# Kernel tuning notes

Measured on AMD Instinct MI355X. Metric: run time of the kernel, lower is better.

Reference implementation:

```python
import jax, jax.numpy as jnp
import numpy as np

N, M, D, DV = 8192, 8192, 64, 64

def setup_inputs() -> dict:
    key = jax.random.key(0)
    kq, kk, kv = jax.random.split(key, 3)
    Q = jax.random.normal(kq, (N, D), dtype=jnp.float32)
    K = jax.random.normal(kk, (M, D), dtype=jnp.float32)
    V = jax.random.normal(kv, (M, DV), dtype=jnp.float32)
    return {"Q": Q, "K": K, "V": V}

def reference(Q, K, V):
    d = K.shape[-1]
    scores = jnp.einsum('nd,md->nm', Q, K) / jnp.sqrt(jnp.float32(d))  # [N, M]
    attn = jax.nn.softmax(scores, axis=-1)
    return attn @ V  # [N, DV]
```

## Files before the change

kernel.cpp:

```cpp
#include <hip/hip_runtime.h>


#define NQ 8192
#define NK 8192

typedef float f32x4 __attribute__((ext_vector_type(4)));
typedef short short8 __attribute__((ext_vector_type(8)));
union U4 { uint4 u; short8 s; };

#define MFMA16 __builtin_amdgcn_mfma_f32_16x16x32_bf16

__device__ __forceinline__ unsigned pk2(float a, float b) {
    unsigned ua = __builtin_bit_cast(unsigned, a);
    unsigned ub = __builtin_bit_cast(unsigned, b);
    ua = (ua + 0x7FFFu + ((ua >> 16) & 1u)) >> 16;
    ub = (ub + 0x7FFFu + ((ub >> 16) & 1u)) & 0xFFFF0000u;
    return ua | ub;
}

__device__ __forceinline__ unsigned pkt(float a, float b) {
    return __builtin_amdgcn_perm(__builtin_bit_cast(unsigned, b),
                                 __builtin_bit_cast(unsigned, a), 0x07060302u);
}

__global__ __launch_bounds__(256)
void prepass(const float* __restrict__ Kg, const float* __restrict__ Vg,
             uint4* __restrict__ Kb4, uint4* __restrict__ Vt4) {
    __shared__ float ld[64 * 33];
    const int t = threadIdx.x, b = blockIdx.x;

    if (b < 256) {
        const int kl = t >> 3, dg = t & 7;
        const int e = kl & 1, i16 = kl >> 1, h = dg >> 2, q = dg & 3;
        const float* gp = Kg + (size_t)(b * 32 + kl) * 64 + dg * 8;
        float4 f0 = *(const float4*)gp;
        float4 f1 = *(const float4*)(gp + 4);
        uint4 o = make_uint4(pk2(f0.x, f0.y), pk2(f0.z, f0.w),
                             pk2(f1.x, f1.y), pk2(f1.z, f1.w));
        Kb4[(size_t)(b * 4 + e * 2 + h) * 64 + i16 * 4 + q] = o;
    } else {
        const int c = b - 256;
        {
            const int key = t >> 3, dg = t & 7;
            const float* gp = Vg + (size_t)(c * 32 + key) * 64 + dg * 8;
            float4 f0 = *(const float4*)gp;
            float4 f1 = *(const float4*)(gp + 4);
            ld[(dg * 8 + 0) * 33 + key] = f0.x;
            ld[(dg * 8 + 1) * 33 + key] = f0.y;
            ld[(dg * 8 + 2) * 33 + key] = f0.z;
            ld[(dg * 8 + 3) * 33 + key] = f0.w;
            ld[(dg * 8 + 4) * 33 + key] = f1.x;
            ld[(dg * 8 + 5) * 33 + key] = f1.y;
            ld[(dg * 8 + 6) * 33 + key] = f1.z;
            ld[(dg * 8 + 7) * 33 + key] = f1.w;
        }
        __syncthreads();
        {
            const int dim = t >> 2, kq = t & 3;
            const int dt = dim >> 4, i16 = dim & 15;
            float v[8];
            #pragma unroll
            for (int j = 0; j < 8; ++j) v[j] = ld[dim * 33 + kq * 8 + j];
            uint4 o = make_uint4(pk2(v[0], v[1]), pk2(v[2], v[3]),
                                 pk2(v[4], v[5]), pk2(v[6], v[7]));
            Vt4[(size_t)(c * 4 + dt) * 64 + i16 * 4 + kq] = o;
        }
    }
}

__global__ __launch_bounds__(512, 1)
void attn_main(const float* __restrict__ Qg,
               const uint4* __restrict__ Kb4,
               const uint4* __restrict__ Vt4,
               float* __restrict__ Opart,
               float* __restrict__ Lpart) {
    __shared__ uint4 shb4[4160];
    float* sF = (float*)shb4;
    unsigned* shu = (unsigned*)shb4;

    const int t = threadIdx.x, w = t >> 6, lane = t & 63;
    const int q = lane >> 4, i16 = lane & 15;
    const int bid = blockIdx.x;
    const int kh = bid & 1;
    const int rg = bid >> 1;
    const int qb0 = rg * 64;
    const int lsl = i16 * 4 + q;
    const int phase = rg & 15;

    const int tpw = ((i16 >> 2) & 1) + 2 * q + 32 * (i16 >> 3);
    const int pp  = i16 & 3;
    const int tpr = (q & 1) + 2 * ((i16 >> 2) & 3) + 8 * (i16 & 3) + 32 * (q >> 1);

    uint4 kfA[4], vfA[4], kfB[4], vfB[4];

#define CBASE(TT) (((kh << 7) + ((((TT) + phase) & 15) * 8 + w)) * 4)

#define LOAD_K(KD, TT)                                                               \
    do {                                                                             \
        const int cb = CBASE(TT);                                                    \
        _Pragma("unroll")                                                            \
        for (int eh = 0; eh < 4; ++eh)                                               \
            (KD)[eh] = Kb4[(size_t)(cb + eh) * 64 + lsl];                            \
    } while (0)

#define LOAD_V(VD, TT)                                                               \
    do {                                                                             \
        const int cb = CBASE(TT);                                                    \
        _Pragma("unroll")                                                            \
        for (int dt = 0; dt < 4; ++dt)                                               \
            (VD)[dt] = Vt4[(size_t)(cb + dt) * 64 + lsl];                            \
    } while (0)

    LOAD_K(kfA, 0);
    LOAD_V(vfA, 0);
    LOAD_K(kfB, 1);

    const float SCL = 0.18033688011112042f;
    short8 aq[4][2];
    #pragma unroll
    for (int rt = 0; rt < 4; ++rt) {
        const float* qp = Qg + (size_t)(qb0 + rt * 16 + i16) * 64 + q * 8;
        float4 f0 = *(const float4*)(qp);
        float4 f1 = *(const float4*)(qp + 4);
        U4 u;
        u.u = make_uint4(pk2(f0.x * SCL, f0.y * SCL), pk2(f0.z * SCL, f0.w * SCL),
                         pk2(f1.x * SCL, f1.y * SCL), pk2(f1.z * SCL, f1.w * SCL));
        aq[rt][0] = u.s;
        f0 = *(const float4*)(qp + 32);
        f1 = *(const float4*)(qp + 36);
        u.u = make_uint4(pk2(f0.x * SCL, f0.y * SCL), pk2(f0.z * SCL, f0.w * SCL),
                         pk2(f1.x * SCL, f1.y * SCL), pk2(f1.z * SCL, f1.w * SCL));
        aq[rt][1] = u.s;
    }

    f32x4 acc[4][4];
    float lsum[4][4];
    #pragma unroll
    for (int rt = 0; rt < 4; ++rt) {
        #pragma unroll
        for (int dt = 0; dt < 4; ++dt) { acc[rt][dt][0]=0.f; acc[rt][dt][1]=0.f; acc[rt][dt][2]=0.f; acc[rt][dt][3]=0.f; }
        #pragma unroll
        for (int r = 0; r < 4; ++r) lsum[rt][r] = 0.f;
    }

#define QKEXP(KD, PAR)                                                               \
    do {                                                                             \
        _Pragma("unroll")                                                            \
        for (int rt = 0; rt < 4; ++rt) {                                             \
            f32x4 s0, s1;                                                            \
            s0[0]=-16.f; s0[1]=-16.f; s0[2]=-16.f; s0[3]=-16.f;                      \
            s1[0]=-16.f; s1[1]=-16.f; s1[2]=-16.f; s1[3]=-16.f;                      \
            U4 u0, u1, u2, u3;                                                       \
            u0.u = (KD)[0]; u1.u = (KD)[1]; u2.u = (KD)[2]; u3.u = (KD)[3];          \
            s0 = MFMA16(aq[rt][0], u0.s, s0, 0, 0, 0);                               \
            s0 = MFMA16(aq[rt][1], u1.s, s0, 0, 0, 0);                               \
            s1 = MFMA16(aq[rt][0], u2.s, s1, 0, 0, 0);                               \
            s1 = MFMA16(aq[rt][1], u3.s, s1, 0, 0, 0);                               \
            const int rbase = (((w * 4 + rt) * 2) + (PAR)) * 256;                    \
            _Pragma("unroll")                                                        \
            for (int r = 0; r < 4; ++r) {                                            \
                float p0 = __builtin_amdgcn_exp2f(s0[r]);                            \
                float p1 = __builtin_amdgcn_exp2f(s1[r]);                            \
                lsum[rt][r] += p0;                                                   \
                lsum[rt][r] += p1;                                                   \
                shu[rbase + (tpw + 8 * r) * 4 + pp] = pkt(p0, p1);                   \
            }                                                                        \
        }                                                                            \
    } while (0)

#define PVS(VD, PAR)                                                                 \
    do {                                                                             \
        U4 ap[4];                                                                    \
        _Pragma("unroll")                                                            \
        for (int rt = 0; rt < 4; ++rt)                                               \
            ap[rt].u = shb4[(((w * 4 + rt) * 2) + (PAR)) * 64 + tpr];                \
        _Pragma("unroll")                                                            \
        for (int dt = 0; dt < 4; ++dt) {                                             \
            U4 bv; bv.u = (VD)[dt];                                                  \
            _Pragma("unroll")                                                        \
            for (int rt = 0; rt < 4; ++rt)                                           \
                acc[rt][dt] = MFMA16(ap[rt].s, bv.s, acc[rt][dt], 0, 0, 0);          \
        }                                                                            \
    } while (0)

    QKEXP(kfA, 0);
    LOAD_K(kfA, 2);
    LOAD_V(vfB, 1);
    #pragma unroll 1
    for (int tt = 1; tt < 15; tt += 2) {
        QKEXP(kfB, 1);
        LOAD_K(kfB, tt + 2);
        PVS(vfA, 0);
        LOAD_V(vfA, tt + 1);
        QKEXP(kfA, 0);
        LOAD_K(kfA, tt + 3);
        PVS(vfB, 1);
        LOAD_V(vfB, tt + 2);
        __builtin_amdgcn_sched_barrier(0);
    }
    QKEXP(kfB, 1);
    PVS(vfA, 0);
    PVS(vfB, 1);

    #pragma unroll
    for (int rt = 0; rt < 4; ++rt)
        #pragma unroll
        for (int r = 0; r < 4; ++r) {
            float v = lsum[rt][r];
            v += __shfl_xor(v, 1);
            v += __shfl_xor(v, 2);
            v += __shfl_xor(v, 4);
            v += __shfl_xor(v, 8);
            lsum[rt][r] = v;
        }

    __syncthreads();
    for (int step = 4; step >= 1; step >>= 1) {
        if (w >= step && w < 2 * step) {
            float* base = sF + (w - step) * 4160;
            #pragma unroll
            for (int rt = 0; rt < 4; ++rt) {
                #pragma unroll
                for (int dt = 0; dt < 4; ++dt)
                    #pragma unroll
                    for (int r = 0; r < 4; ++r)
                        base[(rt * 16 + 4 * q + r) * 64 + dt * 16 + i16] = acc[rt][dt][r];
                if (i16 == 0) {
                    #pragma unroll
                    for (int r = 0; r < 4; ++r) base[4096 + rt * 16 + 4 * q + r] = lsum[rt][r];
                }
            }
        }
        __syncthreads();
        if (w < step) {
            const float* base = sF + w * 4160;
            #pragma unroll
            for (int rt = 0; rt < 4; ++rt) {
                #pragma unroll
                for (int dt = 0; dt < 4; ++dt)
                    #pragma unroll
                    for (int r = 0; r < 4; ++r)
                        acc[rt][dt][r] += base[(rt * 16 + 4 * q + r) * 64 + dt * 16 + i16];
                #pragma unroll
                for (int r = 0; r < 4; ++r) lsum[rt][r] += base[4096 + rt * 16 + 4 * q + r];
            }
        }
        __syncthreads();
    }

    if (w == 0) {
        #pragma unroll
        for (int rt = 0; rt < 4; ++rt) {
            #pragma unroll
            for (int dt = 0; dt < 4; ++dt)
                #pragma unroll
                for (int r = 0; r < 4; ++r) {
                    const int row = qb0 + rt * 16 + 4 * q + r;
                    Opart[((size_t)kh * 8192 + row) * 64 + dt * 16 + i16] = acc[rt][dt][r];
                }
            if (i16 == 0) {
                #pragma unroll
                for (int r = 0; r < 4; ++r)
                    Lpart[kh * 8192 + qb0 + rt * 16 + 4 * q + r] = lsum[rt][r];
            }
        }
    }
}

__global__ __launch_bounds__(256)
void merge(const float* __restrict__ Opart, const float* __restrict__ Lpart,
           float* __restrict__ Og) {
    const int idx = blockIdx.x * 256 + threadIdx.x;
    const int row = idx >> 4, seg = idx & 15;
    const float4 a = *(const float4*)(Opart + (size_t)row * 64 + seg * 4);
    const float4 b = *(const float4*)(Opart + ((size_t)8192 + row) * 64 + seg * 4);
    const float inv = 1.0f / (Lpart[row] + Lpart[8192 + row]);
    float4 o;
    o.x = (a.x + b.x) * inv;
    o.y = (a.y + b.y) * inv;
    o.z = (a.z + b.z) * inv;
    o.w = (a.w + b.w) * inv;
    *(float4*)(Og + (size_t)row * 64 + seg * 4) = o;
}

extern "C" void kernel_launch(void* const* d_in, const int* in_sizes, int n_in,
                              void* d_out, int out_size, void* d_ws, size_t ws_size,
                              hipStream_t stream) {
    const float* Q = (const float*)d_in[0];
    const float* K = (const float*)d_in[1];
    const float* V = (const float*)d_in[2];
    float* O = (float*)d_out;
    char* ws = (char*)d_ws;
    uint4* Kb4   = (uint4*)ws;
    uint4* Vt4   = (uint4*)(ws + (1 << 20));
    float* Opart = (float*)(ws + (2 << 20));
    float* Lpart = (float*)(ws + (6 << 20));
    hipLaunchKernelGGL(prepass, dim3(512), dim3(256), 0, stream, K, V, Kb4, Vt4);
    hipLaunchKernelGGL(attn_main, dim3(256), dim3(512), 0, stream, Q, Kb4, Vt4, Opart, Lpart);
    hipLaunchKernelGGL(merge, dim3(512), dim3(256), 0, stream, Opart, Lpart, O);
}
```

Baseline: 90.37 us.

## Compute transposed scores and shuffle P in registers instead of LDS

The QK product is computed as K·Q^T, so each lane holds scores for one query row. The exp'd probabilities are rearranged into the PV A-operand layout with permlane swap instructions, replacing the LDS write/read round trip. The K and V prepass layouts change to match, and the pipeline is simplified so each tile does QK, exp and PV in one step. This removes LDS traffic and its latency, but the fused per-tile dependency chain may hide less latency than the old split schedule.

```diff
diff --git a/kernel.cpp b/kernel.cpp
--- a/kernel.cpp
+++ b/kernel.cpp
@@ -30,14 +30,16 @@
     const int t = threadIdx.x, b = blockIdx.x;
 
     if (b < 256) {
-        const int kl = t >> 3, dg = t & 7;
-        const int e = kl & 1, i16 = kl >> 1, h = dg >> 2, q = dg & 3;
-        const float* gp = Kg + (size_t)(b * 32 + kl) * 64 + dg * 8;
+        const int f = t >> 6, l = t & 63;
+        const int i16 = l & 15, g = l >> 4;
+        const int row = b * 32 + (f >> 1) * 16 + i16;
+        const int dg = g + (f & 1) * 4;
+        const float* gp = Kg + (size_t)row * 64 + dg * 8;
         float4 f0 = *(const float4*)gp;
         float4 f1 = *(const float4*)(gp + 4);
         uint4 o = make_uint4(pk2(f0.x, f0.y), pk2(f0.z, f0.w),
                              pk2(f1.x, f1.y), pk2(f1.z, f1.w));
-        Kb4[(size_t)(b * 4 + e * 2 + h) * 64 + i16 * 4 + q] = o;
+        Kb4[(size_t)(b * 4 + f) * 64 + l] = o;
     } else {
         const int c = b - 256;
         {
@@ -63,7 +65,7 @@
             for (int j = 0; j < 8; ++j) v[j] = ld[dim * 33 + kq * 8 + j];
             uint4 o = make_uint4(pk2(v[0], v[1]), pk2(v[2], v[3]),
                                  pk2(v[4], v[5]), pk2(v[6], v[7]));
-            Vt4[(size_t)(c * 4 + dt) * 64 + i16 * 4 + kq] = o;
+            Vt4[(size_t)(c * 4 + dt) * 64 + kq * 16 + i16] = o;
         }
     }
 }
@@ -74,9 +76,7 @@
                const uint4* __restrict__ Vt4,
                float* __restrict__ Opart,
                float* __restrict__ Lpart) {
-    __shared__ uint4 shb4[4160];
-    float* sF = (float*)shb4;
-    unsigned* shu = (unsigned*)shb4;
+    __shared__ float sF[4 * 4160];
 
     const int t = threadIdx.x, w = t >> 6, lane = t & 63;
     const int q = lane >> 4, i16 = lane & 15;
@@ -84,12 +84,7 @@
     const int kh = bid & 1;
     const int rg = bid >> 1;
     const int qb0 = rg * 64;
-    const int lsl = i16 * 4 + q;
     const int phase = rg & 15;
-
-    const int tpw = ((i16 >> 2) & 1) + 2 * q + 32 * (i16 >> 3);
-    const int pp  = i16 & 3;
-    const int tpr = (q & 1) + 2 * ((i16 >> 2) & 3) + 8 * (i16 & 3) + 32 * (q >> 1);
 
     uint4 kfA[4], vfA[4], kfB[4], vfB[4];
 
@@ -99,8 +94,8 @@
     do {                                                                             \
         const int cb = CBASE(TT);                                                    \
         _Pragma("unroll")                                                            \
-        for (int eh = 0; eh < 4; ++eh)                                               \
-            (KD)[eh] = Kb4[(size_t)(cb + eh) * 64 + lsl];                            \
+        for (int f = 0; f < 4; ++f)                                                  \
+            (KD)[f] = Kb4[(size_t)(cb + f) * 64 + lane];                             \
     } while (0)
 
 #define LOAD_V(VD, TT)                                                               \
@@ -108,12 +103,11 @@
         const int cb = CBASE(TT);                                                    \
         _Pragma("unroll")                                                            \
         for (int dt = 0; dt < 4; ++dt)                                               \
-            (VD)[dt] = Vt4[(size_t)(cb + dt) * 64 + lsl];                            \
+            (VD)[dt] = Vt4[(size_t)(cb + dt) * 64 + lane];                           \
     } while (0)
 
-    LOAD_K(kfA, 0);
-    LOAD_V(vfA, 0);
-    LOAD_K(kfB, 1);
+    LOAD_K(kfA, 0); LOAD_V(vfA, 0);
+    LOAD_K(kfB, 1); LOAD_V(vfB, 1);
 
     const float SCL = 0.18033688011112042f;
     short8 aq[4][2];
@@ -134,85 +128,69 @@
     }
 
     f32x4 acc[4][4];
-    float lsum[4][4];
+    float lsum[4];
     #pragma unroll
     for (int rt = 0; rt < 4; ++rt) {
         #pragma unroll
         for (int dt = 0; dt < 4; ++dt) { acc[rt][dt][0]=0.f; acc[rt][dt][1]=0.f; acc[rt][dt][2]=0.f; acc[rt][dt][3]=0.f; }
-        #pragma unroll
-        for (int r = 0; r < 4; ++r) lsum[rt][r] = 0.f;
-    }
-
-#define QKEXP(KD, PAR)                                                               \
+        lsum[rt] = 0.f;
+    }
+
+#define TILE(KD, VD)                                                                 \
     do {                                                                             \
         _Pragma("unroll")                                                            \
         for (int rt = 0; rt < 4; ++rt) {                                             \
             f32x4 s0, s1;                                                            \
             s0[0]=-16.f; s0[1]=-16.f; s0[2]=-16.f; s0[3]=-16.f;                      \
             s1[0]=-16.f; s1[1]=-16.f; s1[2]=-16.f; s1[3]=-16.f;                      \
-            U4 u0, u1, u2, u3;                                                       \
-            u0.u = (KD)[0]; u1.u = (KD)[1]; u2.u = (KD)[2]; u3.u = (KD)[3];          \
-            s0 = MFMA16(aq[rt][0], u0.s, s0, 0, 0, 0);                               \
-            s0 = MFMA16(aq[rt][1], u1.s, s0, 0, 0, 0);                               \
-            s1 = MFMA16(aq[rt][0], u2.s, s1, 0, 0, 0);                               \
-            s1 = MFMA16(aq[rt][1], u3.s, s1, 0, 0, 0);                               \
-            const int rbase = (((w * 4 + rt) * 2) + (PAR)) * 256;                    \
+            U4 k0, k1, k2, k3;                                                       \
+            k0.u = (KD)[0]; k1.u = (KD)[1]; k2.u = (KD)[2]; k3.u = (KD)[3];          \
+            s0 = MFMA16(k0.s, aq[rt][0], s0, 0, 0, 0);                               \
+            s0 = MFMA16(k1.s, aq[rt][1], s0, 0, 0, 0);                               \
+            s1 = MFMA16(k2.s, aq[rt][0], s1, 0, 0, 0);                               \
+            s1 = MFMA16(k3.s, aq[rt][1], s1, 0, 0, 0);                               \
+            float p00 = __builtin_amdgcn_exp2f(s0[0]);                               \
+            float p01 = __builtin_amdgcn_exp2f(s0[1]);                               \
+            float p02 = __builtin_amdgcn_exp2f(s0[2]);                               \
+            float p03 = __builtin_amdgcn_exp2f(s0[3]);                               \
+            float p10 = __builtin_amdgcn_exp2f(s1[0]);                               \
+            float p11 = __builtin_amdgcn_exp2f(s1[1]);                               \
+            float p12 = __builtin_amdgcn_exp2f(s1[2]);                               \
+            float p13 = __builtin_amdgcn_exp2f(s1[3]);                               \
+            lsum[rt] += ((p00 + p01) + (p02 + p03)) + ((p10 + p11) + (p12 + p13));   \
+            unsigned w0 = pkt(p00, p01), w1 = pkt(p02, p03);                         \
+            unsigned w2 = pkt(p10, p11), w3 = pkt(p12, p13);                         \
+            asm("v_permlane32_swap_b32 %0, %1" : "+v"(w0), "+v"(w2));                \
+            asm("v_permlane16_swap_b32 %0, %1" : "+v"(w0), "+v"(w2));                \
+            asm("v_permlane32_swap_b32 %0, %1" : "+v"(w1), "+v"(w3));                \
+            asm("v_permlane16_swap_b32 %0, %1" : "+v"(w1), "+v"(w3));                \
+            U4 ap; ap.u = make_uint4(w0, w1, w2, w3);                                \
             _Pragma("unroll")                                                        \
-            for (int r = 0; r < 4; ++r) {                                            \
-                float p0 = __builtin_amdgcn_exp2f(s0[r]);                            \
-                float p1 = __builtin_amdgcn_exp2f(s1[r]);                            \
-                lsum[rt][r] += p0;                                                   \
-                lsum[rt][r] += p1;                                                   \
-                shu[rbase + (tpw + 8 * r) * 4 + pp] = pkt(p0, p1);                   \
+            for (int dt = 0; dt < 4; ++dt) {                                         \
+                U4 bv; bv.u = (VD)[dt];                                              \
+                acc[rt][dt] = MFMA16(ap.s, bv.s, acc[rt][dt], 0, 0, 0);              \
             }                                                                        \
         }                                                                            \
     } while (0)
 
-#define PVS(VD, PAR)                                                                 \
-    do {                                                                             \
-        U4 ap[4];                                                                    \
-        _Pragma("unroll")                                                            \
-        for (int rt = 0; rt < 4; ++rt)                                               \
-            ap[rt].u = shb4[(((w * 4 + rt) * 2) + (PAR)) * 64 + tpr];                \
-        _Pragma("unroll")                                                            \
-        for (int dt = 0; dt < 4; ++dt) {                                             \
-            U4 bv; bv.u = (VD)[dt];                                                  \
-            _Pragma("unroll")                                                        \
-            for (int rt = 0; rt < 4; ++rt)                                           \
-                acc[rt][dt] = MFMA16(ap[rt].s, bv.s, acc[rt][dt], 0, 0, 0);          \
-        }                                                                            \
-    } while (0)
-
-    QKEXP(kfA, 0);
-    LOAD_K(kfA, 2);
-    LOAD_V(vfB, 1);
     #pragma unroll 1
-    for (int tt = 1; tt < 15; tt += 2) {
-        QKEXP(kfB, 1);
-        LOAD_K(kfB, tt + 2);
-        PVS(vfA, 0);
-        LOAD_V(vfA, tt + 1);
-        QKEXP(kfA, 0);
-        LOAD_K(kfA, tt + 3);
-        PVS(vfB, 1);
-        LOAD_V(vfB, tt + 2);
+    for (int tt = 0; tt < 14; tt += 2) {
+        TILE(kfA, vfA);
+        LOAD_K(kfA, tt + 2); LOAD_V(vfA, tt + 2);
+        TILE(kfB, vfB);
+        LOAD_K(kfB, tt + 3); LOAD_V(vfB, tt + 3);
         __builtin_amdgcn_sched_barrier(0);
     }
-    QKEXP(kfB, 1);
-    PVS(vfA, 0);
-    PVS(vfB, 1);
+    TILE(kfA, vfA);
+    TILE(kfB, vfB);
 
     #pragma unroll
-    for (int rt = 0; rt < 4; ++rt)
-        #pragma unroll
-        for (int r = 0; r < 4; ++r) {
-            float v = lsum[rt][r];
-            v += __shfl_xor(v, 1);
-            v += __shfl_xor(v, 2);
-            v += __shfl_xor(v, 4);
-            v += __shfl_xor(v, 8);
-            lsum[rt][r] = v;
-        }
+    for (int rt = 0; rt < 4; ++rt) {
+        float v = lsum[rt];
+        v += __shfl_xor(v, 16);
+        v += __shfl_xor(v, 32);
+        lsum[rt] = v;
+    }
 
     __syncthreads();
     for (int step = 4; step >= 1; step >>= 1) {
@@ -225,10 +203,7 @@
                     #pragma unroll
                     for (int r = 0; r < 4; ++r)
                         base[(rt * 16 + 4 * q + r) * 64 + dt * 16 + i16] = acc[rt][dt][r];
-                if (i16 == 0) {
-                    #pragma unroll
-                    for (int r = 0; r < 4; ++r) base[4096 + rt * 16 + 4 * q + r] = lsum[rt][r];
-                }
+                if (q == 0) base[4096 + rt * 16 + i16] = lsum[rt];
             }
         }
         __syncthreads();
@@ -241,8 +216,7 @@
                     #pragma unroll
                     for (int r = 0; r < 4; ++r)
                         acc[rt][dt][r] += base[(rt * 16 + 4 * q + r) * 64 + dt * 16 + i16];
-                #pragma unroll
-                for (int r = 0; r < 4; ++r) lsum[rt][r] += base[4096 + rt * 16 + 4 * q + r];
+                lsum[rt] += base[4096 + rt * 16 + i16];
             }
         }
         __syncthreads();
@@ -258,11 +232,8 @@
                     const int row = qb0 + rt * 16 + 4 * q + r;
                     Opart[((size_t)kh * 8192 + row) * 64 + dt * 16 + i16] = acc[rt][dt][r];
                 }
-            if (i16 == 0) {
-                #pragma unroll
-                for (int r = 0; r < 4; ++r)
-                    Lpart[kh * 8192 + qb0 + rt * 16 + 4 * q + r] = lsum[rt][r];
-            }
+            if (q == 0)
+                Lpart[kh * 8192 + qb0 + rt * 16 + i16] = lsum[rt];
         }
     }
 }
```

Measured after the change: 86.81 us. -3.9%, faster.
